# Optimization experiments

Measured on AMD Instinct MI355X. Metric: run time of the kernel, lower is better.

## Reference

```python
import jax, jax.numpy as jnp
import numpy as np

ROW, IN_DIM, OUT_DIM, BATCH = 64, 1024, 1024, 512


def setup_inputs() -> dict:
    key = jax.random.key(0)
    k1, k2, k3 = jax.random.split(key, 3)
    x = jax.random.normal(k1, (BATCH, ROW, IN_DIM), dtype=jnp.float32)
    # torch.nn.Linear init: U(-1/sqrt(in_dim), 1/sqrt(in_dim)) for weight and bias
    bound = 1.0 / np.sqrt(IN_DIM)
    W = jax.random.uniform(k2, (ROW, IN_DIM, OUT_DIM), minval=-bound, maxval=bound, dtype=jnp.float32)
    b = jax.random.uniform(k3, (ROW, OUT_DIM), minval=-bound, maxval=bound, dtype=jnp.float32)
    return {"x": x, "W": W, "b": b}


def reference(x, W, b):
    # per-row Linear fused into a single grouped GEMM:
    # out[b, r, o] = sum_i x[b, r, i] * W[r, i, o] + b[r, o]
    return jnp.einsum('bri,rio->bro', x, W) + b[None, :, :]
```

## Files before the change

### kernel.cpp

```cpp
#include <hip/hip_runtime.h>
#include <hip/hip_bf16.h>

#define NROW  64
#define KDIM  1024
#define NDIM  1024

typedef short bf16x8 __attribute__((ext_vector_type(8)));
typedef float f32x4  __attribute__((ext_vector_type(4)));

__device__ __forceinline__ unsigned pk2bf(float lo, float hi) {
  unsigned ulo = __builtin_bit_cast(unsigned, lo) + 0x8000u;
  unsigned uhi = __builtin_bit_cast(unsigned, hi) + 0x8000u;
  return __builtin_amdgcn_perm(uhi, ulo, 0x07060302u);
}

__global__ __launch_bounds__(256) void Group_MLP_kernel(
    const float* __restrict__ x, const float* __restrict__ W,
    const float* __restrict__ bias, float* __restrict__ out) {
  const int g  = blockIdx.x;
  const int r  = g >> 5;
  const int mb = (g >> 3) & 3;
  const int nb = g & 7;
  const int m0 = mb * 128;
  const int n0 = nb * 128;

  const int t    = threadIdx.x;
  const int l    = t & 63;
  const int wave = t >> 6;
  const int wm   = wave >> 1, wn = wave & 1;
  const int lm   = l & 15, quad = l >> 4;

  __shared__ uint4 smem4[1024];
  uint2* s2 = (uint2*)smem4;

  const float* gA[4];
  int lcA[4];
  #pragma unroll
  for (int i = 0; i < 4; ++i) {
    int c = i * 256 + t;
    int p = c >> 1;
    int ma  = ((p >> 6) << 4) | (p & 15);
    int kof = (((p >> 4) & 3) << 3) | ((c & 1) << 2);
    gA[i] = x + (size_t)(m0 + ma) * (NROW * KDIM) + r * KDIM + kof;
    lcA[i] = c;
  }

  const int n4 = t & 31, qh = t >> 5;
  const float* gB = W + (size_t)r * (KDIM * NDIM) + (qh * 4) * NDIM + n0 + n4 * 4;
  const int baseP  = (n4 >> 2) * 64 + ((qh >> 1) & 3) * 16 + (n4 & 3) * 4;
  const int swBase = baseP ^ (n4 >> 2);
  const int hB     = qh & 1;

  int aIdx[4], bIdx[4];
  #pragma unroll
  for (int i = 0; i < 4; ++i) aIdx[i] = (wm * 4 + i) * 64 + l;
  #pragma unroll
  for (int j = 0; j < 4; ++j) {
    int grp = wn * 4 + j;
    bIdx[j] = 512 + grp * 64 + (l ^ grp);
  }

  f32x4 acc[4][4];
  #pragma unroll
  for (int i = 0; i < 4; ++i)
    #pragma unroll
    for (int j = 0; j < 4; ++j)
      acc[i][j] = {0.f, 0.f, 0.f, 0.f};

  float4 pa[4], pb[4];
  #pragma unroll
  for (int i = 0; i < 4; ++i) pa[i] = *(const float4*)(gA[i]);
  #pragma unroll
  for (int j = 0; j < 4; ++j) pb[j] = *(const float4*)(gB + j * NDIM);

  for (int ks = 0; ks < 32; ++ks) {
    __syncthreads();
    #pragma unroll
    for (int i = 0; i < 4; ++i) {
      uint2 v;
      v.x = pk2bf(pa[i].x, pa[i].y);
      v.y = pk2bf(pa[i].z, pa[i].w);
      s2[lcA[i]] = v;
    }
    uint2 ch[4];
    ch[0].x = pk2bf(pb[0].x, pb[1].x); ch[0].y = pk2bf(pb[2].x, pb[3].x);
    ch[1].x = pk2bf(pb[0].y, pb[1].y); ch[1].y = pk2bf(pb[2].y, pb[3].y);
    ch[2].x = pk2bf(pb[0].z, pb[1].z); ch[2].y = pk2bf(pb[2].z, pb[3].z);
    ch[3].x = pk2bf(pb[0].w, pb[1].w); ch[3].y = pk2bf(pb[2].w, pb[3].w);
    #pragma unroll
    for (int c = 0; c < 4; ++c) {
      s2[1024 + ((swBase ^ c) << 1) + hB] = ch[c];
    }
    __syncthreads();
    if (ks < 31) {
      #pragma unroll
      for (int i = 0; i < 4; ++i) { gA[i] += 32; pa[i] = *(const float4*)(gA[i]); }
      gB += 32 * NDIM;
      #pragma unroll
      for (int j = 0; j < 4; ++j) pb[j] = *(const float4*)(gB + j * NDIM);
    }
    bf16x8 af[4], bfr[4];
    #pragma unroll
    for (int i = 0; i < 4; ++i) af[i]  = __builtin_bit_cast(bf16x8, smem4[aIdx[i]]);
    #pragma unroll
    for (int j = 0; j < 4; ++j) bfr[j] = __builtin_bit_cast(bf16x8, smem4[bIdx[j]]);
    #pragma unroll
    for (int i = 0; i < 4; ++i)
      #pragma unroll
      for (int j = 0; j < 4; ++j)
        acc[i][j] = __builtin_amdgcn_mfma_f32_16x16x32_bf16(af[i], bfr[j], acc[i][j], 0, 0, 0);
  }

  const int nColBase = n0 + wn * 64 + lm;
  const int mRowBase = m0 + wm * 64 + quad * 4;
  #pragma unroll
  for (int j = 0; j < 4; ++j) {
    int n = nColBase + j * 16;
    float bv = bias[r * NDIM + n];
    #pragma unroll
    for (int i = 0; i < 4; ++i) {
      int mr = mRowBase + i * 16;
      #pragma unroll
      for (int v = 0; v < 4; ++v) {
        out[(size_t)(mr + v) * (NROW * NDIM) + r * NDIM + n] = acc[i][j][v] + bv;
      }
    }
  }
}

extern "C" void kernel_launch(void* const* d_in, const int* in_sizes, int n_in,
                              void* d_out, int out_size, void* d_ws, size_t ws_size,
                              hipStream_t stream) {
  const float* x    = (const float*)d_in[0];
  const float* W    = (const float*)d_in[1];
  const float* bias = (const float*)d_in[2];
  float* out        = (float*)d_out;
  dim3 grid(64 * 4 * 8), block(256);
  hipLaunchKernelGGL(Group_MLP_kernel, grid, block, 0, stream, x, W, bias, out);
}
```

Baseline: 580.5 us.

## Deepen register prefetch pipeline, remap blocks per XCD, coalesce global loads

Block indices are remapped so that each XCD handles a contiguous range of rows, which should keep each row's W slice local to one L2. Global loads are prefetched two K-steps ahead, and the bf16 conversion for the next step is done after the LDS fragment reads, so it overlaps with the MFMAs. The thread-to-element mapping for A and B loads is changed so adjacent lanes read contiguous memory and LDS write addresses are simpler. In exchange it needs more registers for the extra raw and converted buffers, which may lower occupancy.

```diff
diff --git a/kernel.cpp b/kernel.cpp
--- a/kernel.cpp
+++ b/kernel.cpp
@@ -17,10 +17,12 @@
 __global__ __launch_bounds__(256) void Group_MLP_kernel(
     const float* __restrict__ x, const float* __restrict__ W,
     const float* __restrict__ bias, float* __restrict__ out) {
-  const int g  = blockIdx.x;
-  const int r  = g >> 5;
-  const int mb = (g >> 3) & 3;
-  const int nb = g & 7;
+  const int g   = blockIdx.x;
+  const int xcd = g & 7;
+  const int idx = g >> 3;
+  const int r   = xcd * 8 + (idx >> 5);
+  const int mb  = (idx >> 3) & 3;
+  const int nb  = idx & 7;
   const int m0 = mb * 128;
   const int n0 = nb * 128;
 
@@ -33,23 +35,18 @@
   __shared__ uint4 smem4[1024];
   uint2* s2 = (uint2*)smem4;
 
-  const float* gA[4];
-  int lcA[4];
-  #pragma unroll
-  for (int i = 0; i < 4; ++i) {
-    int c = i * 256 + t;
-    int p = c >> 1;
-    int ma  = ((p >> 6) << 4) | (p & 15);
-    int kof = (((p >> 4) & 3) << 3) | ((c & 1) << 2);
-    gA[i] = x + (size_t)(m0 + ma) * (NROW * KDIM) + r * KDIM + kof;
-    lcA[i] = c;
-  }
+  const int maBase = ((t >> 7) << 4) | ((t >> 1) & 15);
+  const int kof    = (((t >> 5) & 3) << 3) | ((t & 1) << 2);
+  const float* gA0 = x + (size_t)(m0 + maBase) * (NROW * KDIM) + r * KDIM + kof;
+  const size_t ASTRIDE = (size_t)32 * (NROW * KDIM);
 
-  const int n4 = t & 31, qh = t >> 5;
+  const int n4 = (t >> 1) & 31;
+  const int qh = (t & 1) | ((t >> 6) << 1);
   const float* gB = W + (size_t)r * (KDIM * NDIM) + (qh * 4) * NDIM + n0 + n4 * 4;
   const int baseP  = (n4 >> 2) * 64 + ((qh >> 1) & 3) * 16 + (n4 & 3) * 4;
   const int swBase = baseP ^ (n4 >> 2);
   const int hB     = qh & 1;
+  const int bW     = 1024 | (swBase << 1) | hB;
 
   int aIdx[4], bIdx[4];
   #pragma unroll
@@ -67,43 +64,65 @@
     for (int j = 0; j < 4; ++j)
       acc[i][j] = {0.f, 0.f, 0.f, 0.f};
 
-  float4 pa[4], pb[4];
+  float4 rawA[4], rawB[4];
+  uint2  cvtA[4], cvtB[4];
+
   #pragma unroll
-  for (int i = 0; i < 4; ++i) pa[i] = *(const float4*)(gA[i]);
+  for (int i = 0; i < 4; ++i) rawA[i] = *(const float4*)(gA0 + i * ASTRIDE);
   #pragma unroll
-  for (int j = 0; j < 4; ++j) pb[j] = *(const float4*)(gB + j * NDIM);
+  for (int j = 0; j < 4; ++j) rawB[j] = *(const float4*)(gB + j * NDIM);
+
+  #pragma unroll
+  for (int i = 0; i < 4; ++i) {
+    cvtA[i].x = pk2bf(rawA[i].x, rawA[i].y);
+    cvtA[i].y = pk2bf(rawA[i].z, rawA[i].w);
+  }
+  cvtB[0].x = pk2bf(rawB[0].x, rawB[1].x); cvtB[0].y = pk2bf(rawB[2].x, rawB[3].x);
+  cvtB[1].x = pk2bf(rawB[0].y, rawB[1].y); cvtB[1].y = pk2bf(rawB[2].y, rawB[3].y);
+  cvtB[2].x = pk2bf(rawB[0].z, rawB[1].z); cvtB[2].y = pk2bf(rawB[2].z, rawB[3].z);
+  cvtB[3].x = pk2bf(rawB[0].w, rawB[1].w); cvtB[3].y = pk2bf(rawB[2].w, rawB[3].w);
+
+  gA0 += 32;
+  gB  += 32 * NDIM;
+  #pragma unroll
+  for (int i = 0; i < 4; ++i) rawA[i] = *(const float4*)(gA0 + i * ASTRIDE);
+  #pragma unroll
+  for (int j = 0; j < 4; ++j) rawB[j] = *(const float4*)(gB + j * NDIM);
 
   for (int ks = 0; ks < 32; ++ks) {
     __syncthreads();
     #pragma unroll
-    for (int i = 0; i < 4; ++i) {
-      uint2 v;
-      v.x = pk2bf(pa[i].x, pa[i].y);
-      v.y = pk2bf(pa[i].z, pa[i].w);
-      s2[lcA[i]] = v;
-    }
-    uint2 ch[4];
-    ch[0].x = pk2bf(pb[0].x, pb[1].x); ch[0].y = pk2bf(pb[2].x, pb[3].x);
-    ch[1].x = pk2bf(pb[0].y, pb[1].y); ch[1].y = pk2bf(pb[2].y, pb[3].y);
-    ch[2].x = pk2bf(pb[0].z, pb[1].z); ch[2].y = pk2bf(pb[2].z, pb[3].z);
-    ch[3].x = pk2bf(pb[0].w, pb[1].w); ch[3].y = pk2bf(pb[2].w, pb[3].w);
+    for (int i = 0; i < 4; ++i) s2[i * 256 + t] = cvtA[i];
     #pragma unroll
-    for (int c = 0; c < 4; ++c) {
-      s2[1024 + ((swBase ^ c) << 1) + hB] = ch[c];
-    }
+    for (int c = 0; c < 4; ++c) s2[bW ^ (c << 1)] = cvtB[c];
     __syncthreads();
-    if (ks < 31) {
-      #pragma unroll
-      for (int i = 0; i < 4; ++i) { gA[i] += 32; pa[i] = *(const float4*)(gA[i]); }
-      gB += 32 * NDIM;
-      #pragma unroll
-      for (int j = 0; j < 4; ++j) pb[j] = *(const float4*)(gB + j * NDIM);
-    }
+
     bf16x8 af[4], bfr[4];
     #pragma unroll
     for (int i = 0; i < 4; ++i) af[i]  = __builtin_bit_cast(bf16x8, smem4[aIdx[i]]);
     #pragma unroll
     for (int j = 0; j < 4; ++j) bfr[j] = __builtin_bit_cast(bf16x8, smem4[bIdx[j]]);
+
+    if (ks < 31) {
+      #pragma unroll
+      for (int i = 0; i < 4; ++i) {
+        cvtA[i].x = pk2bf(rawA[i].x, rawA[i].y);
+        cvtA[i].y = pk2bf(rawA[i].z, rawA[i].w);
+      }
+      cvtB[0].x = pk2bf(rawB[0].x, rawB[1].x); cvtB[0].y = pk2bf(rawB[2].x, rawB[3].x);
+      cvtB[1].x = pk2bf(rawB[0].y, rawB[1].y); cvtB[1].y = pk2bf(rawB[2].y, rawB[3].y);
+      cvtB[2].x = pk2bf(rawB[0].z, rawB[1].z); cvtB[2].y = pk2bf(rawB[2].z, rawB[3].z);
+      cvtB[3].x = pk2bf(rawB[0].w, rawB[1].w); cvtB[3].y = pk2bf(rawB[2].w, rawB[3].w);
+      if (ks < 30) {
+        gA0 += 32;
+        gB  += 32 * NDIM;
+        #pragma unroll
+        for (int i = 0; i < 4; ++i) rawA[i] = *(const float4*)(gA0 + i * ASTRIDE);
+        #pragma unroll
+        for (int j = 0; j < 4; ++j) rawB[j] = *(const float4*)(gB + j * NDIM);
+      }
+    }
+
     #pragma unroll
     for (int i = 0; i < 4; ++i)
       #pragma unroll
```

Result: faster. 566.4 us (-2.4%).
